# Kernel optimization log

Measured on AMD Instinct MI355X. Metric: run time of the kernel, lower is better.

The kernel has to match this reference:

```python
import jax, jax.numpy as jnp
from jax import lax
import numpy as np

B, EMB, HEADS, LAYERS = 32, 512, 8, 4
SEQ_JD, TOK = 200, 50

def _mask_lg(S):
    # Faithful vectorization of CoKEModel.mask_lg (True = masked)
    m = np.ones((B, HEADS, S, S), dtype=bool)
    rows = np.arange(S)[:, None]
    cols = np.clip(rows - 5 + np.arange(10)[None, :], 0, S - 1)  # window=10, offset -5..4
    for h in range(6):  # local_len = 6 local-window heads
        m[:, h, rows, cols] = False
    m[0, 6:] = False          # global heads unmasked only for batch 0 (faithful to source)
    m[:, :, 0, :] = False     # CLS row attends everywhere
    return m

def _ln_free(x):
    # CoKEModel.layer_norm: no affine, eps=1e-12, rsqrt form
    mu = jnp.mean(x, axis=-1, keepdims=True)
    sx = x - mu
    v = jnp.mean(sx * sx, axis=-1, keepdims=True)
    return sx * jnp.sqrt(1.0 / (v + 1e-12))

def _ln(x, g, b):
    mu = jnp.mean(x, axis=-1, keepdims=True)
    sx = x - mu
    v = jnp.mean(sx * sx, axis=-1, keepdims=True)
    return sx / jnp.sqrt(v + 1e-5) * g + b

def _textcnn(tokens, emb, cws, cbs, fw, fb):
    e = emb[tokens]                        # (N, 50, 1024)
    x = jnp.transpose(e, (0, 2, 1))        # (N, 1024, 50): embed dim as channels
    pooled = []
    for W, b in zip(cws, cbs):             # W: (100, k, 1024)
        rhs = jnp.transpose(W, (0, 2, 1))  # (100, 1024, k)
        y = lax.conv_general_dilated(x, rhs, (1,), 'VALID', dimension_numbers=('NCH', 'OIH', 'NCH'))
        y = jax.nn.relu(y + b[None, :, None])
        pooled.append(jnp.max(y, axis=2))  # global max-pool over time
    return jnp.concatenate(pooled, axis=1) @ fw.T + fb   # (N, 512)

def _encoder(x, mask, wq, bq, wk, bk, wv, bv, wo, bo, l1g, l1b, fw1, fb1, fw2, fb2, l2g, l2b):
    Bb, S, D = x.shape
    dh = D // HEADS
    scale = 1.0 / (dh ** 0.5)
    for l in range(LAYERS):
        q = (x @ wq[l].T + bq[l]).reshape(Bb, S, HEADS, dh)
        k = (x @ wk[l].T + bk[l]).reshape(Bb, S, HEADS, dh)
        v = (x @ wv[l].T + bv[l]).reshape(Bb, S, HEADS, dh)
        s = jnp.einsum('bshd,bthd->bhst', q, k) * scale
        s = jnp.where(mask, -1e9, s)
        a = jax.nn.softmax(s, axis=-1)
        c = jnp.einsum('bhst,bthd->bshd', a, v).reshape(Bb, S, D)
        x = _ln(x + c @ wo[l].T + bo[l], l1g[l], l1b[l])
        h = jax.nn.relu(x @ fw1[l].T + fb1[l])
        x = _ln(x + h @ fw2[l].T + fb2[l], l2g[l], l2b[l])
    return x

def _contrastive(im, s, margin=0.02):
    sc = im @ s.T
    d = jnp.diag(sc)
    cs = jnp.maximum(margin + sc - d[:, None], 0.0)
    ci = jnp.maximum(margin + sc - d[None, :], 0.0)
    eye = jnp.eye(sc.shape[0], dtype=bool)
    cs = jnp.where(eye, 0.0, cs)
    ci = jnp.where(eye, 0.0, ci)
    return jnp.sum(cs) + jnp.sum(ci)

def _forward(floats, src, mask101, mask200):
    (user_info, label_similarity, emb_tc, cw1, cb1, cw2, cb2, cw3, cb3, tfw, tfb,
     wq, bq, wk, bk, wv, bv, wo, bo, l1g, l1b, fw1, fb1, fw2, fb2, l2g, l2b,
     fc1w, fc1b, fc2w, fc2b, fc3w, fc3b, fc4w, fc4b, pscale, pbias) = floats
    cws, cbs = (cw1, cw2, cw3), (cb1, cb2, cb3)
    enc = (wq, bq, wk, bk, wv, bv, wo, bo, l1g, l1b, fw1, fb1, fw2, fb2, l2g, l2b)

    # ---- first pass: first 100 JDs + global CLS token ----
    s1 = _textcnn(src[:, :100].reshape(-1, TOK), emb_tc, cws, cbs, tfw, tfb).reshape(B, 100, EMB)
    s1 = _ln_free(s1)
    s1 = jnp.concatenate([jnp.zeros((B, 1, EMB), s1.dtype), s1], axis=1)  # (B, 101, EMB)
    p = _encoder(s1, mask101, *enc)
    p = jax.nn.gelu(p @ fc1w.T + fc1b, approximate=False)
    p = _ln_free(p)
    p = p * pscale[:, :p.shape[1]] + pbias[:, :p.shape[1]]
    p = p @ fc2w.T + fc2b                      # (B, 101, 204)
    cls_e, tok = p[:, :1], p[:, 1:]
    P = tok @ fc3w.T + fc3b                    # (B, 100, 204)
    clsIII = cls_e @ fc3w.T + fc3b             # (B, 1, 204)
    SLl = jnp.einsum('bsm,bsn->bmn', P, P)     # P^T @ P
    SL_hat = label_similarity[None] + 0.4 * SLl
    outIII = jnp.squeeze(clsIII @ SL_hat, axis=1)  # (B, 204)

    # ---- second pass: all 200 JDs ----
    s2 = _textcnn(src.reshape(-1, TOK), emb_tc, cws, cbs, tfw, tfb).reshape(B, SEQ_JD, EMB)
    s2 = _ln_free(s2)
    ap = _encoder(s2, mask200, *enc)
    ap = jax.nn.gelu(ap @ fc1w.T + fc1b, approximate=False)
    ap = _ln_free(ap)
    ap = ap * pscale[:, :SEQ_JD] + pbias[:, :SEQ_JD]
    p1 = ap @ fc2w.T + fc2b                    # (B, 200, 204)

    nn_ = SEQ_JD // 100  # = 2 neighbors
    eps = 1e-6
    skl_rows, seuc_rows = [], []
    for i in range(nn_):
        # NOTE: faithful to source slicing bug: [i : (i+1)*100]
        c1 = jax.nn.softmax(jnp.mean(p1[:, i:(i + 1) * 100], axis=1), axis=-1)
        a1 = jax.nn.softmax(jnp.mean(ap[:, i:(i + 1) * 100], axis=1), axis=-1)
        rk, re = [], []
        for j in range(nn_):
            c2 = jax.nn.softmax(jnp.mean(p1[:, j:(j + 1) * 100], axis=1), axis=-1)
            a2 = jax.nn.softmax(jnp.mean(ap[:, j:(j + 1) * 100], axis=1), axis=-1)
            rk.append(jnp.sum((c1 + eps) * jnp.log((c1 + eps) / (c2 + eps)), axis=-1))
            re.append(jnp.sqrt(jnp.sum((a1 - a2) ** 2, axis=-1) + 1e-12))
        skl_rows.append(jnp.stack(rk, axis=-1))
        seuc_rows.append(jnp.stack(re, axis=-1))
    skl = jnp.stack(skl_rows, axis=1).reshape(B, -1) * 10.0
    seuc = jnp.stack(seuc_rows, axis=1).reshape(B, -1)
    skl = jax.nn.softmax(skl, axis=-1)
    seuc = jax.nn.softmax(seuc, axis=-1)
    loss_sims = jnp.mean(jnp.sum((skl + eps) * jnp.log((skl + eps) / (seuc + eps)), axis=-1))

    cls4m = jnp.squeeze(cls_e, axis=1)
    user4m = user_info @ fc4w.T + fc4b
    nrm = lambda x: x / jnp.maximum(jnp.linalg.norm(x, axis=1, keepdims=True), 1e-12)
    match = _contrastive(nrm(cls4m), nrm(user4m))

    return (jax.nn.softmax(outIII, axis=-1),
            jax.nn.softmax(cls_e, axis=-1),
            loss_sims * 100000.0,
            match * 0.01)

def setup_inputs():
    key = jax.random.key(0)
    kit = iter(jax.random.split(key, 48))
    def nrm(shape, s=0.02):
        return jax.random.normal(next(kit), shape, jnp.float32) * s
    d = {}
    d['src'] = jax.random.randint(next(kit), (B, SEQ_JD, TOK), 0, 20000)
    d['user_info'] = nrm((B, 142), 1.0)
    d['label_similarity'] = nrm((204, 204))
    d['emb_tc'] = nrm((20000, 1024)).at[0].set(0.0)  # padding_idx=0 row zeroed
    d['cw1'], d['cb1'] = nrm((100, 1, 1024)), jnp.zeros((100,), jnp.float32)
    d['cw2'], d['cb2'] = nrm((100, 2, 1024)), jnp.zeros((100,), jnp.float32)
    d['cw3'], d['cb3'] = nrm((100, 3, 1024)), jnp.zeros((100,), jnp.float32)
    d['tfw'], d['tfb'] = nrm((512, 300)), jnp.zeros((512,), jnp.float32)
    d['wq'], d['bq'] = nrm((LAYERS, EMB, EMB)), jnp.zeros((LAYERS, EMB), jnp.float32)
    d['wk'], d['bk'] = nrm((LAYERS, EMB, EMB)), jnp.zeros((LAYERS, EMB), jnp.float32)
    d['wv'], d['bv'] = nrm((LAYERS, EMB, EMB)), jnp.zeros((LAYERS, EMB), jnp.float32)
    d['wo'], d['bo'] = nrm((LAYERS, EMB, EMB)), jnp.zeros((LAYERS, EMB), jnp.float32)
    d['l1g'], d['l1b'] = jnp.ones((LAYERS, EMB), jnp.float32), jnp.zeros((LAYERS, EMB), jnp.float32)
    d['fw1'], d['fb1'] = nrm((LAYERS, 2048, EMB)), jnp.zeros((LAYERS, 2048), jnp.float32)
    d['fw2'], d['fb2'] = nrm((LAYERS, EMB, 2048)), jnp.zeros((LAYERS, EMB), jnp.float32)
    d['l2g'], d['l2b'] = jnp.ones((LAYERS, EMB), jnp.float32), jnp.zeros((LAYERS, EMB), jnp.float32)
    d['fc1w'], d['fc1b'] = nrm((EMB, EMB)), jnp.zeros((EMB,), jnp.float32)
    d['fc2w'], d['fc2b'] = nrm((204, EMB)), jnp.zeros((204,), jnp.float32)
    d['fc3w'], d['fc3b'] = nrm((204, 204)), jnp.zeros((204,), jnp.float32)
    d['fc4w'], d['fc4b'] = nrm((204, 142)), jnp.zeros((204,), jnp.float32)
    d['pscale'] = jnp.ones((B, 300, EMB), jnp.float32)
    d['pbias'] = jnp.zeros((B, 300, EMB), jnp.float32)
    d['mask101'] = jnp.asarray(_mask_lg(101))
    d['mask200'] = jnp.asarray(_mask_lg(SEQ_JD))
    return d

def reference(src, user_info, label_similarity, emb_tc, cw1, cb1, cw2, cb2, cw3, cb3, tfw, tfb, wq, bq, wk, bk, wv, bv, wo, bo, l1g, l1b, fw1, fb1, fw2, fb2, l2g, l2b, fc1w, fc1b, fc2w, fc2b, fc3w, fc3b, fc4w, fc4b, pscale, pbias, mask101, mask200):
    floats = (user_info, label_similarity, emb_tc, cw1, cb1, cw2, cb2, cw3, cb3, tfw, tfb,
              wq, bq, wk, bk, wv, bv, wo, bo, l1g, l1b, fw1, fb1, fw2, fb2, l2g, l2b,
              fc1w, fc1b, fc2w, fc2b, fc3w, fc3b, fc4w, fc4b, pscale, pbias)
    return _forward(floats, src, mask101, mask200)
```

## Files before the change

kernel.cpp:

```cpp
#include <hip/hip_runtime.h>
#include <math.h>

#define EMB 512
#define HEADS 8
#define NLAYERS 4
#define NB 32
#define SEQ 200
#define TOKN 50
#define DH 64
#define FFND 2048
#define NCLS 204
#define VC 640
#define KD 1024
#define CCH 8
#define CROWS (6400/CCH)
#define CM (CROWS*TOKN)
#define MSEG 16
#define CMT ((CM + 127) / 128)
#define CNT (VC / 128)
#define CT  (CMT * CNT)

typedef __attribute__((ext_vector_type(8))) short v8s;
typedef __attribute__((ext_vector_type(4))) float v4f;
typedef unsigned short ushort_t;
// ... 449 lines not shown
        #pragma unroll
        for (int e = 0; e < 8; e++){
          int k = k0 + bkq + e;
          he[e] = (k < K) ? bph[k0 + e] : (ushort_t)0;
          le[e] = (k < K) ? bpl[k0 + e] : (ushort_t)0;
        }
        h0 = *(uint4*)&he[0];
        l0 = *(uint4*)&le[0];
      }
      *(uint4*)&Bhi[brow][bkq] = h0;
      *(uint4*)&Blo[brow][bkq] = l0;
    }
    __syncthreads();

    v8s ah[4], al[4];
    #pragma unroll
    for (int mi = 0; mi < 4; mi++){
      ah[mi] = *(const v8s*)&Ahi[wm + mi*16 + lcol][lq*8];
      al[mi] = *(const v8s*)&Alo[wm + mi*16 + lcol][lq*8];
    }
    #pragma unroll
    for (int ni = 0; ni < 2; ni++){
      v8s bh = *(const v8s*)&Bhi[wn + ni*16 + lcol][lq*8];
      v8s bl = *(const v8s*)&Blo[wn + ni*16 + lcol][lq*8];
      #pragma unroll
      for (int mi = 0; mi < 4; mi++){
        acc[mi][ni] = __builtin_amdgcn_mfma_f32_16x16x32_bf16(ah[mi], bh, acc[mi][ni], 0, 0, 0);
        acc[mi][ni] = __builtin_amdgcn_mfma_f32_16x16x32_bf16(al[mi], bh, acc[mi][ni], 0, 0, 0);
        acc[mi][ni] = __builtin_amdgcn_mfma_f32_16x16x32_bf16(ah[mi], bl, acc[mi][ni], 0, 0, 0);
      }
    }
    __syncthreads();
  }

  #pragma unroll
  for (int ni = 0; ni < 2; ni++){
    int n = n0 + wn + ni*16 + lcol;
    if (n >= N) continue;
    float bv = (ks == 1 || slice == 0) ? bias[n] : 0.f;
    #pragma unroll
    for (int mi = 0; mi < 4; mi++){
      int mbase = m0 + wm + mi*16 + lq*4;
      #pragma unroll
      for (int rg = 0; rg < 4; rg++){
        int m = mbase + rg;
        if (m >= M) continue;
        float v = acc[mi][ni][rg] + bv;
        if (ks == 1){
          if (act == 1) v = fmaxf(v, 0.f);
          else if (act == 2) v = 0.5f * v * (1.f + erff(v * 0.70710678118654752f));
          C[(size_t)m * ldc + n] = v;
        } else {
          atomicAdd(&C[(size_t)m * ldc + n], v);
        }
      }
    }
  }
}

__global__ __launch_bounds__(256, 2) void gemm_mfma_kernel(
    const float* __restrict__ A, const float* __restrict__ W,
    const float* __restrict__ bias, float* __restrict__ C,
    int M, int N, int K, int ldc, int act)
{
  __shared__ ushort_t Ahi[128][40];
  __shared__ ushort_t Alo[128][40];
  __shared__ ushort_t Bhi[128][40];
  __shared__ ushort_t Blo[128][40];

  const int tid = threadIdx.x;
  const int m0 = blockIdx.y * 128, n0 = blockIdx.x * 128;
  const int wave = tid >> 6, lane = tid & 63;
  const int wm = (wave >> 1) * 64, wn = (wave & 1) * 64;
  const int lcol = lane & 15, lq = lane >> 4;

  v4f acc[4][4];
  #pragma unroll
  for (int i = 0; i < 4; i++)
    #pragma unroll
    for (int j = 0; j < 4; j++) acc[i][j] = (v4f){0.f, 0.f, 0.f, 0.f};

  const int srow = tid >> 1;
  const int skh  = (tid & 1) * 16;

  for (int k0 = 0; k0 < K; k0 += 32){
    {
      float av[16];
      int m = m0 + srow;
      const float* ap = A + (size_t)m * K + k0 + skh;
      bool mok = (m < M);
      if (mok && (k0 + 32 <= K)){
        #pragma unroll
        for (int q = 0; q < 4; q++){
          float4 f = ((const float4*)ap)[q];
          av[q*4+0]=f.x; av[q*4+1]=f.y; av[q*4+2]=f.z; av[q*4+3]=f.w;
        }
      } else {
        #pragma unroll
        for (int e = 0; e < 16; e++){
          int k = k0 + skh + e;
          av[e] = (mok && k < K) ? ap[e] : 0.f;
        }
      }
      uint4 uh[2], ul[2];
      #pragma unroll
      for (int h = 0; h < 2; h++){
        unsigned hw[8], lw[8];
        #pragma unroll
        for (int e = 0; e < 8; e++){
          float x = av[h*8+e];
          unsigned u = __float_as_uint(x);
          float hf = __uint_as_float(u & 0xFFFF0000u);
          hw[e] = u >> 16;
          lw[e] = f2bu(x - hf);
        }
        uh[h] = make_uint4(hw[0]|(hw[1]<<16), hw[2]|(hw[3]<<16), hw[4]|(hw[5]<<16), hw[6]|(hw[7]<<16));
        ul[h] = make_uint4(lw[0]|(lw[1]<<16), lw[2]|(lw[3]<<16), lw[4]|(lw[5]<<16), lw[6]|(lw[7]<<16));
      }
      *(uint4*)&Ahi[srow][skh]     = uh[0];
      *(uint4*)&Ahi[srow][skh + 8] = uh[1];
      *(uint4*)&Alo[srow][skh]     = ul[0];
      *(uint4*)&Alo[srow][skh + 8] = ul[1];
    }
    {
      float bv[16];
      int n = n0 + srow;
      const float* bp = W + (size_t)n * K + k0 + skh;
      bool nok = (n < N);
      if (nok && (k0 + 32 <= K)){
        #pragma unroll
        for (int q = 0; q < 4; q++){
          float4 f = ((const float4*)bp)[q];
          bv[q*4+0]=f.x; bv[q*4+1]=f.y; bv[q*4+2]=f.z; bv[q*4+3]=f.w;
        }
      } else {
        #pragma unroll
        for (int e = 0; e < 16; e++){
          int k = k0 + skh + e;
          bv[e] = (nok && k < K) ? bp[e] : 0.f;
        }
      }
      uint4 uh[2], ul[2];
      #pragma unroll
      for (int h = 0; h < 2; h++){
        unsigned hw[8], lw[8];
        #pragma unroll
        for (int e = 0; e < 8; e++){
          float x = bv[h*8+e];
          unsigned u = __float_as_uint(x);
          float hf = __uint_as_float(u & 0xFFFF0000u);
          hw[e] = u >> 16;
          lw[e] = f2bu(x - hf);
        }
        uh[h] = make_uint4(hw[0]|(hw[1]<<16), hw[2]|(hw[3]<<16), hw[4]|(hw[5]<<16), hw[6]|(hw[7]<<16));
        ul[h] = make_uint4(lw[0]|(lw[1]<<16), lw[2]|(lw[3]<<16), lw[4]|(lw[5]<<16), lw[6]|(lw[7]<<16));
      }
      *(uint4*)&Bhi[srow][skh]     = uh[0];
      *(uint4*)&Bhi[srow][skh + 8] = uh[1];
      *(uint4*)&Blo[srow][skh]     = ul[0];
      *(uint4*)&Blo[srow][skh + 8] = ul[1];
    }
    __syncthreads();

    v8s ah[4], al[4];
    #pragma unroll
    for (int mi = 0; mi < 4; mi++){
      ah[mi] = *(const v8s*)&Ahi[wm + mi*16 + lcol][lq*8];
      al[mi] = *(const v8s*)&Alo[wm + mi*16 + lcol][lq*8];
    }
    #pragma unroll
    for (int ni = 0; ni < 4; ni++){
      v8s bh = *(const v8s*)&Bhi[wn + ni*16 + lcol][lq*8];
      v8s bl = *(const v8s*)&Blo[wn + ni*16 + lcol][lq*8];
      #pragma unroll
      for (int mi = 0; mi < 4; mi++){
        acc[mi][ni] = __builtin_amdgcn_mfma_f32_16x16x32_bf16(ah[mi], bh, acc[mi][ni], 0, 0, 0);
        acc[mi][ni] = __builtin_amdgcn_mfma_f32_16x16x32_bf16(al[mi], bh, acc[mi][ni], 0, 0, 0);
        acc[mi][ni] = __builtin_amdgcn_mfma_f32_16x16x32_bf16(ah[mi], bl, acc[mi][ni], 0, 0, 0);
      }
    }
    __syncthreads();
  }

  #pragma unroll
  for (int ni = 0; ni < 4; ni++){
    int n = n0 + wn + ni*16 + lcol;
    if (n >= N) continue;
    float bv = bias[n];
    #pragma unroll
    for (int mi = 0; mi < 4; mi++){
      int mbase = m0 + wm + mi*16 + lq*4;
      #pragma unroll
      for (int rg = 0; rg < 4; rg++){
        int m = mbase + rg;
        if (m >= M) continue;
        float v = acc[mi][ni][rg] + bv;
        if (act == 1) v = fmaxf(v, 0.f);
        else if (act == 2) v = 0.5f * v * (1.f + erff(v * 0.70710678118654752f));
        C[(size_t)m * ldc + n] = v;
      }
    }
  }
}

__global__ __launch_bounds__(256) void gemm_kernel(
    const float* __restrict__ A, const float* __restrict__ W,
    const float* __restrict__ bias, float* __restrict__ C,
    int M, int N, int K, int act)
{
  __shared__ float As[16][64];
  __shared__ float Ws[16][64];
  const int tid = threadIdx.x;
  const int m0 = blockIdx.y * 64, n0 = blockIdx.x * 64;
  const int lr = tid >> 2;
  const int lk = (tid & 3) * 4;
  const int tx = tid & 15, ty = tid >> 4;
  float cc[4][4];
  #pragma unroll
  for (int i = 0; i < 4; i++)
    #pragma unroll
    for (int j = 0; j < 4; j++) cc[i][j] = 0.f;

  for (int k0 = 0; k0 < K; k0 += 16){
    #pragma unroll
    for (int i = 0; i < 4; i++){
      int k = k0 + lk + i;
      int m = m0 + lr;
      As[lk + i][lr] = (m < M && k < K) ? A[(size_t)m * K + k] : 0.f;
      int n = n0 + lr;
      Ws[lk + i][lr] = (n < N && k < K) ? W[(size_t)n * K + k] : 0.f;
    }
    __syncthreads();
    #pragma unroll
    for (int kk = 0; kk < 16; kk++){
      float4 a = *(const float4*)&As[kk][ty * 4];
      float4 b = *(const float4*)&Ws[kk][tx * 4];
      float av[4] = {a.x, a.y, a.z, a.w};
      float bv[4] = {b.x, b.y, b.z, b.w};
      #pragma unroll
      for (int i = 0; i < 4; i++)
        #pragma unroll
        for (int j = 0; j < 4; j++) cc[i][j] = fmaf(av[i], bv[j], cc[i][j]);
    }
    __syncthreads();
  }

  #pragma unroll
  for (int i = 0; i < 4; i++){
    int m = m0 + ty * 4 + i;
    if (m >= M) continue;
    #pragma unroll
    for (int j = 0; j < 4; j++){
      int n = n0 + tx * 4 + j;
      if (n >= N) continue;
      float v = cc[i][j] + bias[n];
      if (act == 1) v = fmaxf(v, 0.f);
      else if (act == 2) v = 0.5f * v * (1.f + erff(v * 0.70710678118654752f));
      C[(size_t)m * N + n] = v;
    }
  }
}

__global__ __launch_bounds__(256) void ln_kernel(
    const float* __restrict__ X, const float* __restrict__ Res,
    const float* __restrict__ g, const float* __restrict__ bta,
    const float* __restrict__ pscale, const float* __restrict__ pbias,
    float* __restrict__ Y, int S, float eps)
{
  __shared__ float red[8];
  const int r = blockIdx.x, tid = threadIdx.x;
  size_t o0 = (size_t)r * EMB + tid;
  size_t o1 = o0 + 256;
  float v0 = X[o0] + (Res ? Res[o0] : 0.f);
  float v1 = X[o1] + (Res ? Res[o1] : 0.f);
  float tot = block_reduce(v0 + v1, red, 4, false);
  float mu = tot * (1.f / 512.f);
  float s0 = v0 - mu, s1 = v1 - mu;
  float var = block_reduce(s0 * s0 + s1 * s1, red, 4, false) * (1.f / 512.f);
  float rs = 1.f / sqrtf(var + eps);
  float y0 = s0 * rs, y1 = s1 * rs;
  if (g){
    y0 = y0 * g[tid] + bta[tid];
    y1 = y1 * g[tid + 256] + bta[tid + 256];
  }
  if (pscale){
    int b = r / S, t = r % S;
    size_t po = ((size_t)(b * 300 + t)) * EMB;
    y0 = y0 * pscale[po + tid] + pbias[po + tid];
    y1 = y1 * pscale[po + tid + 256] + pbias[po + tid + 256];
  }
  Y[o0] = y0;
  Y[o1] = y1;
}

__global__ __launch_bounds__(64) void vmean_kernel(const float* __restrict__ qkv,
                                                   float* __restrict__ vm, int S){
  int bh = blockIdx.x; int b = bh >> 3, h = bh & 7; int d = threadIdx.x;
  const float* vr = qkv + (size_t)(b * S) * 1536 + 1024 + h * DH + d;
  float s = 0.f;
  for (int j = 0; j < S; j++) s += vr[(size_t)j * 1536];
  vm[bh * DH + d] = s / (float)S;
}

__global__ __launch_bounds__(64) void attn_kernel(
    const float* __restrict__ qkv, const float* __restrict__ vm,
    float* __restrict__ Ctx, int S)
{
  __shared__ float qv[DH];
  __shared__ float sc[SEQ];
  __shared__ float wts[16];
  const int tid = threadIdx.x;
  const int blk = blockIdx.x;
  const int i = blk % S;
  const int bh = blk / S;
  const int h = bh % HEADS;
  const int b = bh / HEADS;
  const size_t rowoff = ((size_t)(b * S + i)) * 1536 + h * DH;
  const size_t coff = ((size_t)(b * S + i)) * EMB + h * DH;
  const bool rowall = (i == 0) || (b == 0 && h >= 6);

  if (rowall){
    qv[tid] = qkv[rowoff + tid];
    __syncthreads();
    for (int j = tid; j < S; j += 64){
      const float* kr = qkv + ((size_t)(b * S + j)) * 1536 + 512 + h * DH;
      float d = 0.f;
      #pragma unroll
      for (int d4 = 0; d4 < 16; d4++){
        float4 kk = *(const float4*)(kr + d4 * 4);
        d = fmaf(qv[d4*4+0], kk.x, d);
        d = fmaf(qv[d4*4+1], kk.y, d);
        d = fmaf(qv[d4*4+2], kk.z, d);
        d = fmaf(qv[d4*4+3], kk.w, d);
      }
      sc[j] = d * 0.125f;
    }
    __syncthreads();
    float mx = -INFINITY;
    for (int j = tid; j < S; j += 64) mx = fmaxf(mx, sc[j]);
    #pragma unroll
    for (int o = 32; o > 0; o >>= 1) mx = fmaxf(mx, __shfl_down(mx, o, 64));
    mx = __shfl(mx, 0, 64);
    float sm = 0.f;
    for (int j = tid; j < S; j += 64){ float e = expf(sc[j] - mx); sc[j] = e; sm += e; }
    #pragma unroll
    for (int o = 32; o > 0; o >>= 1) sm += __shfl_down(sm, o, 64);
    sm = __shfl(sm, 0, 64);
    float inv = 1.f / sm;
    __syncthreads();
    float a_ = 0.f;
    const float* vr = qkv + ((size_t)(b * S)) * 1536 + 1024 + h * DH + tid;
    for (int j = 0; j < S; j++) a_ = fmaf(sc[j], vr[(size_t)j * 1536], a_);
    Ctx[coff + tid] = a_ * inv;
  } else if (h < 6){
    qv[tid] = qkv[rowoff + tid];
    __syncthreads();
    const int lo = max(0, i - 5), hi = min(S - 1, i + 4);
    const int cnt = hi - lo + 1;
    float s = -INFINITY;
    if (tid < cnt){
      const float* kr = qkv + ((size_t)(b * S + lo + tid)) * 1536 + 512 + h * DH;
      float d = 0.f;
      #pragma unroll
      for (int d4 = 0; d4 < 16; d4++){
        float4 kk = *(const float4*)(kr + d4 * 4);
        d = fmaf(qv[d4*4+0], kk.x, d);
        d = fmaf(qv[d4*4+1], kk.y, d);
        d = fmaf(qv[d4*4+2], kk.z, d);
        d = fmaf(qv[d4*4+3], kk.w, d);
      }
      s = d * 0.125f;
    }
    float mx = s;
    #pragma unroll
    for (int o = 8; o > 0; o >>= 1) mx = fmaxf(mx, __shfl_xor(mx, o, 16));
    float e = (tid < cnt) ? expf(s - mx) : 0.f;
    float sm = e;
    #pragma unroll
    for (int o = 8; o > 0; o >>= 1) sm += __shfl_xor(sm, o, 16);
    if (tid < 16) wts[tid] = e / sm;
    __syncthreads();
    float a_ = 0.f;
    const float* vr = qkv + ((size_t)(b * S + lo)) * 1536 + 1024 + h * DH + tid;
    for (int j = 0; j < cnt; j++) a_ = fmaf(wts[j], vr[(size_t)j * 1536], a_);
    Ctx[coff + tid] = a_;
  } else {
    Ctx[coff + tid] = vm[(b * HEADS + h) * DH + tid];
  }
}

__global__ void buildx1_kernel(const float* __restrict__ base, float* __restrict__ x1){
  int idx = blockIdx.x * 256 + threadIdx.x;
  if (idx >= NB * 101 * EMB) return;
  int e = idx & 511;
  int bt = idx >> 9;
  int t = bt % 101, b = bt / 101;
  x1[idx] = (t == 0) ? 0.f : base[((size_t)(b * SEQ + t - 1)) * EMB + e];
}

__global__ void extract_kernel(const float* __restrict__ p2, float* __restrict__ clsE, float* __restrict__ tok){
  int idx = blockIdx.x * 256 + threadIdx.x;
  if (idx >= NB * 101 * NCLS) return;
  int n = idx % NCLS;
  int bt = idx / NCLS;
  int t = bt % 101, b = bt / 101;
  float v = p2[idx];
  if (t == 0) clsE[b * NCLS + n] = v;
  else tok[((size_t)(b * 100 + t - 1)) * NCLS + n] = v;
}

__global__ void zero_kernel(float* p){ if (threadIdx.x == 0) p[0] = 0.f; }

__global__ __launch_bounds__(256) void slhat_kernel(
    const float* __restrict__ P, const float* __restrict__ ls, float* __restrict__ SLh)
{
  int bm = blockIdx.x;
  int b = bm / NCLS, m = bm % NCLS;
  int n = threadIdx.x;
  if (n >= NCLS) return;
  const float* Pb = P + (size_t)b * 100 * NCLS;
  float s = 0.f;
  for (int t = 0; t < 100; t++) s = fmaf(Pb[t * NCLS + m], Pb[t * NCLS + n], s);
  SLh[((size_t)bm) * NCLS + n] = ls[m * NCLS + n] + 0.4f * s;
}

__global__ __launch_bounds__(256) void outIII_kernel(
    const float* __restrict__ cls3, const float* __restrict__ SLh, float* __restrict__ o3)
{
  int b = blockIdx.x, n = threadIdx.x;
  if (n >= NCLS) return;
  float s = 0.f;
  for (int m = 0; m < NCLS; m++)
    s = fmaf(cls3[b * NCLS + m], SLh[((size_t)(b * NCLS + m)) * NCLS + n], s);
  o3[b * NCLS + n] = s;
}

__global__ __launch_bounds__(256) void softmax_out_kernel(const float* __restrict__ X, float* __restrict__ O, int n){
  __shared__ float red[8];
  int r = blockIdx.x, tid = threadIdx.x;
  float mx = -INFINITY;
  for (int j = tid; j < n; j += 256) mx = fmaxf(mx, X[(size_t)r * n + j]);
  mx = block_reduce(mx, red, 4, true);
  float sm = 0.f;
  for (int j = tid; j < n; j += 256) sm += expf(X[(size_t)r * n + j] - mx);
  sm = block_reduce(sm, red, 4, false);
  for (int j = tid; j < n; j += 256) O[(size_t)r * n + j] = expf(X[(size_t)r * n + j] - mx) / sm;
}

__global__ __launch_bounds__(256) void normalize_kernel(
    const float* __restrict__ clsE, const float* __restrict__ u4,
    float* __restrict__ imn, float* __restrict__ sn)
{
  __shared__ float red[8];
  int r = blockIdx.x, tid = threadIdx.x;
  const float* s = (r < NB) ? (clsE + (size_t)r * NCLS) : (u4 + (size_t)(r - NB) * NCLS);
  float* d = (r < NB) ? (imn + (size_t)r * NCLS) : (sn + (size_t)(r - NB) * NCLS);
  float v = (tid < NCLS) ? s[tid] : 0.f;
  float ss = block_reduce(v * v, red, 4, false);
  float nrm = fmaxf(sqrtf(ss), 1e-12f);
  if (tid < NCLS) d[tid] = v / nrm;
}

__global__ __launch_bounds__(1024) void contrastive_kernel(
    const float* __restrict__ imn, const float* __restrict__ sn, float* __restrict__ out)
{
  __shared__ float sc[NB][NB];
  __shared__ float red[16];
  int tid = threadIdx.x;
  int i = tid >> 5, j = tid & 31;
  float d = 0.f;
  for (int c = 0; c < NCLS; c++) d = fmaf(imn[i * NCLS + c], sn[j * NCLS + c], d);
  sc[i][j] = d;
  __syncthreads();
  float di = sc[i][i], dj = sc[j][j];
  float v = 0.f;
  if (i != j)
    v = fmaxf(0.02f + sc[i][j] - di, 0.f) + fmaxf(0.02f + sc[i][j] - dj, 0.f);
  #pragma unroll
  for (int o = 32; o > 0; o >>= 1) v += __shfl_down(v, o, 64);
  if ((tid & 63) == 0) red[tid >> 6] = v;
  __syncthreads();
  if (tid == 0){
    float s = 0.f;
    for (int w = 0; w < 16; w++) s += red[w];
    out[13057] = s * 0.01f;
  }
}

__global__ __launch_bounds__(256) void means_part_kernel(
    const float* __restrict__ p1, const float* __restrict__ ap,
    float* __restrict__ part)
{
  const int blk = blockIdx.x;
  const int bi = blk / MSEG, seg = blk % MSEG;
  const int b = bi >> 1, i = bi & 1;
  const int start = i;
  const int cnt = (i == 0) ? 100 : 199;
  const int per = (cnt + MSEG - 1) / MSEG;
  const int r0 = seg * per;
  const int r1 = min(r0 + per, cnt);
  float* dst = part + (size_t)blk * 720;
  for (int c = threadIdx.x; c < NCLS + EMB; c += 256){
    float s = 0.f;
    if (c < NCLS){
      for (int rr = r0; rr < r1; rr++)
        s += p1[((size_t)(b * SEQ + start + rr)) * NCLS + c];
    } else {
      int cc = c - NCLS;
      for (int rr = r0; rr < r1; rr++)
        s += ap[((size_t)(b * SEQ + start + rr)) * EMB + cc];
    }
    dst[c] = s;
  }
}

__global__ __launch_bounds__(256) void means_final_kernel(
    const float* __restrict__ part, float* __restrict__ mp, float* __restrict__ ma)
{
  const int bi = blockIdx.x;
  const int i = bi & 1;
  const float icnt = (i == 0) ? (1.f / 100.f) : (1.f / 199.f);
  for (int c = threadIdx.x; c < NCLS + EMB; c += 256){
    float s = 0.f;
    #pragma unroll
    for (int g = 0; g < MSEG; g++)
      s += part[((size_t)(bi * MSEG + g)) * 720 + c];
    if (c < NCLS) mp[(size_t)bi * NCLS + c] = s * icnt;
    else          ma[(size_t)bi * EMB + (c - NCLS)] = s * icnt;
  }
}

__global__ __launch_bounds__(64) void klfinal_kernel(
    const float* __restrict__ cbuf, const float* __restrict__ abuf, float* __restrict__ acc)
{
  const int b = blockIdx.x, lane = threadIdx.x;
  float rk[4], re[4];
  #pragma unroll
  for (int pr = 0; pr < 4; pr++){
    int i = pr >> 1, j = pr & 1;
    const float* c1 = cbuf + ((size_t)(b * 2 + i)) * NCLS;
    const float* c2 = cbuf + ((size_t)(b * 2 + j)) * NCLS;
    float s = 0.f;
    for (int n = lane; n < NCLS; n += 64){
      float x = c1[n] + 1e-6f, y = c2[n] + 1e-6f;
      s += x * logf(x / y);
    }
    #pragma unroll
    for (int o = 32; o > 0; o >>= 1) s += __shfl_down(s, o, 64);
    rk[pr] = __shfl(s, 0, 64);
    const float* a1 = abuf + ((size_t)(b * 2 + i)) * EMB;
    const float* a2 = abuf + ((size_t)(b * 2 + j)) * EMB;
    float s2 = 0.f;
    for (int n = lane; n < EMB; n += 64){
      float dd = a1[n] - a2[n];
      s2 += dd * dd;
    }
    #pragma unroll
    for (int o = 32; o > 0; o >>= 1) s2 += __shfl_down(s2, o, 64);
    re[pr] = sqrtf(__shfl(s2, 0, 64) + 1e-12f);
  }
  if (lane == 0){
    float sk[4], se[4];
    float mk = -INFINITY, me = -INFINITY;
    for (int p = 0; p < 4; p++){
      sk[p] = rk[p] * 10.f;
      mk = fmaxf(mk, sk[p]);
      se[p] = re[p];
      me = fmaxf(me, se[p]);
    }
    float ssk = 0.f, sse = 0.f;
    for (int p = 0; p < 4; p++){ sk[p] = expf(sk[p] - mk); ssk += sk[p]; se[p] = expf(se[p] - me); sse += se[p]; }
    float loss = 0.f;
    for (int p = 0; p < 4; p++){
      float x = sk[p] / ssk + 1e-6f, y = se[p] / sse + 1e-6f;
      loss += x * logf(x / y);
    }
    atomicAdd(acc, loss);
  }
}

__global__ void finalize_kernel(const float* __restrict__ acc, float* __restrict__ out){
  if (threadIdx.x == 0) out[13056] = acc[0] * (100000.f / 32.f);
}

extern "C" void kernel_launch(void* const* d_in, const int* in_sizes, int n_in,
                              void* d_out, int out_size, void* d_ws, size_t ws_size,
                              hipStream_t stream)
{
  (void)in_sizes; (void)n_in; (void)out_size;
  const int*   src  = (const int*)  d_in[0];
  const float* user_info = (const float*)d_in[1];
  const float* ls   = (const float*)d_in[2];
  const float* emb  = (const float*)d_in[3];
  const float* cw1  = (const float*)d_in[4];  const float* cb1 = (const float*)d_in[5];
  const float* cw2  = (const float*)d_in[6];  const float* cb2 = (const float*)d_in[7];
  const float* cw3  = (const float*)d_in[8];  const float* cb3 = (const float*)d_in[9];
  const float* tfw  = (const float*)d_in[10]; const float* tfb = (const float*)d_in[11];
  const float* wq   = (const float*)d_in[12]; const float* bq  = (const float*)d_in[13];
  const float* wk   = (const float*)d_in[14]; const float* bk  = (const float*)d_in[15];
  const float* wv   = (const float*)d_in[16]; const float* bv  = (const float*)d_in[17];
  const float* wo   = (const float*)d_in[18]; const float* bo  = (const float*)d_in[19];
  const float* l1g  = (const float*)d_in[20]; const float* l1b = (const float*)d_in[21];
  const float* fw1  = (const float*)d_in[22]; const float* fb1 = (const float*)d_in[23];
  const float* fw2  = (const float*)d_in[24]; const float* fb2 = (const float*)d_in[25];
  const float* l2g  = (const float*)d_in[26]; const float* l2b = (const float*)d_in[27];
  const float* fc1w = (const float*)d_in[28]; const float* fc1b= (const float*)d_in[29];
  const float* fc2w = (const float*)d_in[30]; const float* fc2b= (const float*)d_in[31];
  const float* fc3w = (const float*)d_in[32]; const float* fc3b= (const float*)d_in[33];
  const float* fc4w = (const float*)d_in[34]; const float* fc4b= (const float*)d_in[35];
  const float* pscale = (const float*)d_in[36];
  const float* pbias  = (const float*)d_in[37];
  float* out = (float*)d_out;
  float* ws = (float*)d_ws;

  size_t off = 0;
  auto alloc = [&](size_t n){ float* p = ws + off; off += ((n + 3) & ~(size_t)3); return p; };
  float* base = alloc(6400ULL * EMB);
  float* x1   = alloc((size_t)NB * 101 * EMB);
  float* qkv  = alloc(6400ULL * 1536);
  float* ctx  = alloc(6400ULL * EMB);
  float* proj = alloc(6400ULL * EMB);
  float* hb   = alloc(6400ULL * FFND);
  float* p2   = alloc(6400ULL * NCLS);
  float* clsE = alloc((size_t)NB * NCLS);
  float* tok  = alloc(3200ULL * NCLS);
  float* Pb   = alloc(3200ULL * NCLS);
  float* cls3 = alloc((size_t)NB * NCLS);
  float* SLh  = alloc((size_t)NB * NCLS * NCLS);
  float* o3   = alloc((size_t)NB * NCLS);
  float* u4   = alloc((size_t)NB * NCLS);
  float* imn  = alloc((size_t)NB * NCLS);
  float* sn   = alloc((size_t)NB * NCLS);
  float* mp   = alloc(64ULL * NCLS);
  float* ma   = alloc(64ULL * EMB);
  float* cbf  = alloc(64ULL * NCLS);
  float* abf  = alloc(64ULL * EMB);
  float* lacc = alloc(4);
  float* vmb  = alloc((size_t)NB * HEADS * DH);
  ushort_t* Wb = (ushort_t*)alloc((size_t)VC * KD / 2);
  float* tfwT = alloc(300ULL * EMB);
  float* bqkv = alloc(4ULL * 1536);
  ushort_t* embb = (ushort_t*)qkv;
  const size_t OQKV = 0, OWO = 3145728, OF1 = 4194304, OF2 = 8388608;
  const size_t OC1 = 12582912, OC2 = 12845056, OC3 = 12949504, WTOT = 12991120;
  ushort_t* WhiA = (ushort_t*)alloc((WTOT + 1) / 2);
  ushort_t* WloA = (ushort_t*)alloc((WTOT + 1) / 2);
  const bool presplit = (off * sizeof(float) <= ws_size);

  auto gemm_f32 = [&](const float* A, const float* W, const float* bi, float* C,
                      int M, int N, int K, int act){
    dim3 g((N + 63) / 64, (M + 63) / 64);
    gemm_kernel<<<g, 256, 0, stream>>>(A, W, bi, C, M, N, K, act);
  };
  auto gemm_fly = [&](const float* A, const float* W, const float* bi, float* C,
                      int M, int N, int K, int ldc, int act){
    dim3 g((N + 127) / 128, (M + 127) / 128);
    gemm_mfma_kernel<<<g, 256, 0, stream>>>(A, W, bi, C, M, N, K, ldc, act);
  };
  auto gemm_pre = [&](const float* A, size_t woff, const float* bi, float* C,
                      int M, int N, int K, int ldc, int act){
    int mt = (M + 127) / 128;
    if (N <= 512){
      int nt = (N + 63) / 64;
      int tiles = mt * nt;
      int ks = 1;
      if (act == 0){
        while (ks < 8 && tiles * ks * 2 <= 2048 && K / (ks * 2) >= 128) ks *= 2;
      }
      if (ks > 1){
        size_t n4 = ((size_t)M * N) / 4;
        int zg = (int)min((n4 + 255) / 256, (size_t)2048);
        zerobuf_kernel<<<zg, 256, 0, stream>>>(C, n4);
      }
      gemm_mfma_pre64_kernel<<<tiles * ks, 256, 0, stream>>>(
          A, WhiA + woff, WloA + woff, bi, C, M, N, K, ldc, act, mt, nt, ks);
    } else {
      int nt = (N + 127) / 128;
      gemm_mfma_pre_kernel<<<mt * nt, 256, 0, stream>>>(
          A, WhiA + woff, WloA + woff, bi, C, M, N, K, ldc, act, mt, nt);
    }
  };
  auto split = [&](const float* srcw, size_t woff, int n){
    split_kernel<<<(n / 4 + 255) / 256, 256, 0, stream>>>(srcw, WhiA + woff, WloA + woff, n);
  };

  prep_w_kernel<<<(VC * KD / 4 + 255) / 256, 256, 0, stream>>>(cw1, cw2, cw3, Wb);
  prep_embbf_kernel<<<(int)((20000ULL * KD / 4 + 255) / 256), 256, 0, stream>>>(emb, embb);
  prep_tfwT_kernel<<<(300 * EMB + 255) / 256, 256, 0, stream>>>(tfw, tfwT);
  if (presplit){
    for (int l = 0; l < NLAYERS; l++){
      split(wq + (size_t)l * 262144, OQKV + (size_t)l * 786432,          262144);
      split(wk + (size_t)l * 262144, OQKV + (size_t)l * 786432 + 262144, 262144);
      split(wv + (size_t)l * 262144, OQKV + (size_t)l * 786432 + 524288, 262144);
      split(wo + (size_t)l * 262144, OWO + (size_t)l * 262144, 262144);
      split(fw1 + (size_t)l * 1048576, OF1 + (size_t)l * 1048576, 1048576);
      split(fw2 + (size_t)l * 1048576, OF2 + (size_t)l * 1048576, 1048576);
    }
    split(fc1w, OC1, 262144);
    split(fc2w, OC2, NCLS * EMB);
    split(fc3w, OC3, NCLS * NCLS);
    qkvbias_kernel<<<4, 256, 0, stream>>>(bq, bk, bv, bqkv);
  }

  for (int c = 0; c < CCH; c++){
    conv_gemm_kernel<<<CT, 256, 0, stream>>>(
        src + (size_t)c * CM, embb, Wb, (ushort_t*)hb, CM);
    pool_fc_kernel<<<CROWS, 256, 0, stream>>>(
        (ushort_t*)hb, tfwT, cb1, cb2, cb3, tfb, base + (size_t)c * CROWS * EMB);
  }
  buildx1_kernel<<<(NB * 101 * EMB + 255) / 256, 256, 0, stream>>>(base, x1);

  auto encoder = [&](float* x, int S){
    int M = NB * S;
    for (int l = 0; l < NLAYERS; l++){
      if (presplit){
        gemm_pre(x, OQKV + (size_t)l * 786432, bqkv + l * 1536, qkv, M, 1536, EMB, 1536, 0);
      } else {
        gemm_fly(x, wq + (size_t)l * EMB * EMB, bq + l * EMB, qkv,        M, EMB, EMB, 1536, 0);
        gemm_fly(x, wk + (size_t)l * EMB * EMB, bk + l * EMB, qkv + 512,  M, EMB, EMB, 1536, 0);
        gemm_fly(x, wv + (size_t)l * EMB * EMB, bv + l * EMB, qkv + 1024, M, EMB, EMB, 1536, 0);
      }
      vmean_kernel<<<NB * HEADS, 64, 0, stream>>>(qkv, vmb, S);
      attn_kernel<<<NB * HEADS * S, 64, 0, stream>>>(qkv, vmb, ctx, S);
      if (presplit) gemm_pre(ctx, OWO + (size_t)l * 262144, bo + l * EMB, proj, M, EMB, EMB, EMB, 0);
      else gemm_fly(ctx, wo + (size_t)l * EMB * EMB, bo + l * EMB, proj, M, EMB, EMB, EMB, 0);
      ln_kernel<<<M, 256, 0, stream>>>(proj, x, l1g + l * EMB, l1b + l * EMB, nullptr, nullptr, x, S, 1e-5f);
      if (presplit) gemm_pre(x, OF1 + (size_t)l * 1048576, fb1 + l * FFND, hb, M, FFND, EMB, FFND, 1);
      else gemm_fly(x, fw1 + (size_t)l * FFND * EMB, fb1 + l * FFND, hb, M, FFND, EMB, FFND, 1);
      if (presplit) gemm_pre(hb, OF2 + (size_t)l * 1048576, fb2 + l * EMB, proj, M, EMB, FFND, EMB, 0);
      else gemm_fly(hb, fw2 + (size_t)l * EMB * FFND, fb2 + l * EMB, proj, M, EMB, FFND, EMB, 0);
      ln_kernel<<<M, 256, 0, stream>>>(proj, x, l2g + l * EMB, l2b + l * EMB, nullptr, nullptr, x, S, 1e-5f);
    }
    if (presplit) gemm_pre(x, OC1, fc1b, ctx, M, EMB, EMB, EMB, 2);
    else gemm_fly(x, fc1w, fc1b, ctx, M, EMB, EMB, EMB, 2);
    ln_kernel<<<M, 256, 0, stream>>>(ctx, nullptr, nullptr, nullptr, pscale, pbias, ctx, S, 1e-12f);
    if (presplit) gemm_pre(ctx, OC2, fc2b, p2, M, NCLS, EMB, NCLS, 0);
    else gemm_fly(ctx, fc2w, fc2b, p2, M, NCLS, EMB, NCLS, 0);
  };

  encoder(x1, 101);
  extract_kernel<<<(NB * 101 * NCLS + 255) / 256, 256, 0, stream>>>(p2, clsE, tok);
  if (presplit) gemm_pre(tok, OC3, fc3b, Pb, 3200, NCLS, NCLS, NCLS, 0);
  else gemm_fly(tok, fc3w, fc3b, Pb, 3200, NCLS, NCLS, NCLS, 0);
  gemm_f32(clsE, fc3w, fc3b, cls3, NB, NCLS, NCLS, 0);
  slhat_kernel<<<NB * NCLS, 256, 0, stream>>>(Pb, ls, SLh);
  outIII_kernel<<<NB, 256, 0, stream>>>(cls3, SLh, o3);
  softmax_out_kernel<<<NB, 256, 0, stream>>>(o3, out, NCLS);
  softmax_out_kernel<<<NB, 256, 0, stream>>>(clsE, out + NB * NCLS, NCLS);
  gemm_f32(user_info, fc4w, fc4b, u4, NB, NCLS, 142, 0);
  normalize_kernel<<<64, 256, 0, stream>>>(clsE, u4, imn, sn);
  contrastive_kernel<<<1, 1024, 0, stream>>>(imn, sn, out);

  encoder(base, SEQ);
  zero_kernel<<<1, 64, 0, stream>>>(lacc);
  means_part_kernel<<<64 * MSEG, 256, 0, stream>>>(p2, ctx, hb);
  means_final_kernel<<<64, 256, 0, stream>>>(hb, mp, ma);
  softmax_out_kernel<<<64, 256, 0, stream>>>(mp, cbf, NCLS);
  softmax_out_kernel<<<64, 256, 0, stream>>>(ma, abf, EMB);
  klfinal_kernel<<<NB, 64, 0, stream>>>(cbf, abf, lacc);
  finalize_kernel<<<1, 64, 0, stream>>>(lacc, out);
}
```

Before: 5.308 ms.

## Split attention into full-row, banded, and mean-fill kernels; limit split-K to large K

The single divergent attention kernel is split into three specialised kernels. One handles the rows that attend to every position (CLS rows, plus the global heads of batch 0). One handles the local 10-wide window with one wavefront per row, four rows per block, keeping scores in registers and reducing dot products with cross-lane shuffles. The third copies the precomputed V-mean for masked global-head rows. This removes block-level branch divergence and the many tiny 64-thread blocks, at the cost of two extra launches per layer. Split-K in the small-N GEMM path is now restricted to K>=1024, which avoids the zero-fill kernel and atomic accumulation for the K=512 GEMMs.

```diff
diff --git a/kernel.cpp b/kernel.cpp
--- a/kernel.cpp
+++ b/kernel.cpp
@@ -775,91 +775,108 @@
   vm[bh * DH + d] = s / (float)S;
 }
 
-__global__ __launch_bounds__(64) void attn_kernel(
-    const float* __restrict__ qkv, const float* __restrict__ vm,
-    float* __restrict__ Ctx, int S)
+__global__ __launch_bounds__(64) void attn_full_kernel(
+    const float* __restrict__ qkv, float* __restrict__ Ctx, int S)
 {
   __shared__ float qv[DH];
   __shared__ float sc[SEQ];
-  __shared__ float wts[16];
   const int tid = threadIdx.x;
   const int blk = blockIdx.x;
-  const int i = blk % S;
-  const int bh = blk / S;
-  const int h = bh % HEADS;
-  const int b = bh / HEADS;
+  int b, h, i;
+  if (blk < NB * HEADS){ b = blk >> 3; h = blk & 7; i = 0; }
+  else {
+    int idx = blk - NB * HEADS;
+    b = 0; h = 6 + idx / (S - 1); i = 1 + idx % (S - 1);
+  }
   const size_t rowoff = ((size_t)(b * S + i)) * 1536 + h * DH;
   const size_t coff = ((size_t)(b * S + i)) * EMB + h * DH;
-  const bool rowall = (i == 0) || (b == 0 && h >= 6);
-
-  if (rowall){
-    qv[tid] = qkv[rowoff + tid];
-    __syncthreads();
-    for (int j = tid; j < S; j += 64){
-      const float* kr = qkv + ((size_t)(b * S + j)) * 1536 + 512 + h * DH;
-      float d = 0.f;
-      #pragma unroll
-      for (int d4 = 0; d4 < 16; d4++){
-        float4 kk = *(const float4*)(kr + d4 * 4);
-        d = fmaf(qv[d4*4+0], kk.x, d);
-        d = fmaf(qv[d4*4+1], kk.y, d);
-        d = fmaf(qv[d4*4+2], kk.z, d);
-        d = fmaf(qv[d4*4+3], kk.w, d);
-      }
-      sc[j] = d * 0.125f;
-    }
-    __syncthreads();
-    float mx = -INFINITY;
-    for (int j = tid; j < S; j += 64) mx = fmaxf(mx, sc[j]);
-    #pragma unroll
-    for (int o = 32; o > 0; o >>= 1) mx = fmaxf(mx, __shfl_down(mx, o, 64));
-    mx = __shfl(mx, 0, 64);
-    float sm = 0.f;
-    for (int j = tid; j < S; j += 64){ float e = expf(sc[j] - mx); sc[j] = e; sm += e; }
-    #pragma unroll
-    for (int o = 32; o > 0; o >>= 1) sm += __shfl_down(sm, o, 64);
-    sm = __shfl(sm, 0, 64);
-    float inv = 1.f / sm;
-    __syncthreads();
-    float a_ = 0.f;
-    const float* vr = qkv + ((size_t)(b * S)) * 1536 + 1024 + h * DH + tid;
-    for (int j = 0; j < S; j++) a_ = fmaf(sc[j], vr[(size_t)j * 1536], a_);
-    Ctx[coff + tid] = a_ * inv;
-  } else if (h < 6){
-    qv[tid] = qkv[rowoff + tid];
-    __syncthreads();
-    const int lo = max(0, i - 5), hi = min(S - 1, i + 4);
-    const int cnt = hi - lo + 1;
-    float s = -INFINITY;
-    if (tid < cnt){
-      const float* kr = qkv + ((size_t)(b * S + lo + tid)) * 1536 + 512 + h * DH;
-      float d = 0.f;
-      #pragma unroll
-      for (int d4 = 0; d4 < 16; d4++){
-        float4 kk = *(const float4*)(kr + d4 * 4);
-        d = fmaf(qv[d4*4+0], kk.x, d);
-        d = fmaf(qv[d4*4+1], kk.y, d);
-        d = fmaf(qv[d4*4+2], kk.z, d);
-        d = fmaf(qv[d4*4+3], kk.w, d);
-      }
-      s = d * 0.125f;
-    }
-    float mx = s;
-    #pragma unroll
-    for (int o = 8; o > 0; o >>= 1) mx = fmaxf(mx, __shfl_xor(mx, o, 16));
-    float e = (tid < cnt) ? expf(s - mx) : 0.f;
-    float sm = e;
-    #pragma unroll
-    for (int o = 8; o > 0; o >>= 1) sm += __shfl_xor(sm, o, 16);
-    if (tid < 16) wts[tid] = e / sm;
-    __syncthreads();
-    float a_ = 0.f;
-    const float* vr = qkv + ((size_t)(b * S + lo)) * 1536 + 1024 + h * DH + tid;
-    for (int j = 0; j < cnt; j++) a_ = fmaf(wts[j], vr[(size_t)j * 1536], a_);
-    Ctx[coff + tid] = a_;
-  } else {
-    Ctx[coff + tid] = vm[(b * HEADS + h) * DH + tid];
-  }
+
+  qv[tid] = qkv[rowoff + tid];
+  __syncthreads();
+  for (int j = tid; j < S; j += 64){
+    const float* kr = qkv + ((size_t)(b * S + j)) * 1536 + 512 + h * DH;
+    float d = 0.f;
+    #pragma unroll
+    for (int d4 = 0; d4 < 16; d4++){
+      float4 kk = *(const float4*)(kr + d4 * 4);
+      d = fmaf(qv[d4*4+0], kk.x, d);
+      d = fmaf(qv[d4*4+1], kk.y, d);
+      d = fmaf(qv[d4*4+2], kk.z, d);
+      d = fmaf(qv[d4*4+3], kk.w, d);
+    }
+    sc[j] = d * 0.125f;
+  }
+  __syncthreads();
+  float mx = -INFINITY;
+  for (int j = tid; j < S; j += 64) mx = fmaxf(mx, sc[j]);
+  #pragma unroll
+  for (int o = 32; o > 0; o >>= 1) mx = fmaxf(mx, __shfl_down(mx, o, 64));
+  mx = __shfl(mx, 0, 64);
+  float sm = 0.f;
+  for (int j = tid; j < S; j += 64){ float e = expf(sc[j] - mx); sc[j] = e; sm += e; }
+  #pragma unroll
+  for (int o = 32; o > 0; o >>= 1) sm += __shfl_down(sm, o, 64);
+  sm = __shfl(sm, 0, 64);
+  float inv = 1.f / sm;
+  __syncthreads();
+  float a_ = 0.f;
+  const float* vr = qkv + ((size_t)(b * S)) * 1536 + 1024 + h * DH + tid;
+  for (int j = 0; j < S; j++) a_ = fmaf(sc[j], vr[(size_t)j * 1536], a_);
+  Ctx[coff + tid] = a_ * inv;
+}
+
+__global__ __launch_bounds__(256) void attn_band_kernel(
+    const float* __restrict__ qkv, float* __restrict__ Ctx, int S)
+{
+  const int rows = NB * 6 * (S - 1);
+  const int r = blockIdx.x * 4 + (threadIdx.x >> 6);
+  const int lane = threadIdx.x & 63;
+  if (r >= rows) return;
+  const int i = 1 + r % (S - 1);
+  const int q_ = r / (S - 1);
+  const int h = q_ % 6, b = q_ / 6;
+  const float* base = qkv + (size_t)(b * S) * 1536;
+  const float qd = base[(size_t)i * 1536 + h * DH + lane];
+  const int lo = max(0, i - 5), hi = min(S - 1, i + 4);
+  const int cnt = hi - lo + 1;
+
+  float sc_r[10];
+  #pragma unroll
+  for (int jj = 0; jj < 10; jj++){
+    float p = 0.f;
+    if (jj < cnt) p = qd * base[(size_t)(lo + jj) * 1536 + 512 + h * DH + lane];
+    #pragma unroll
+    for (int o = 32; o > 0; o >>= 1) p += __shfl_xor(p, o, 64);
+    sc_r[jj] = (jj < cnt) ? p * 0.125f : -INFINITY;
+  }
+  float mx = sc_r[0];
+  #pragma unroll
+  for (int jj = 1; jj < 10; jj++) mx = fmaxf(mx, sc_r[jj]);
+  float sm = 0.f;
+  #pragma unroll
+  for (int jj = 0; jj < 10; jj++){ sc_r[jj] = expf(sc_r[jj] - mx); sm += sc_r[jj]; }
+  const float inv = 1.f / sm;
+  float a_ = 0.f;
+  #pragma unroll
+  for (int jj = 0; jj < 10; jj++){
+    if (jj < cnt) a_ = fmaf(sc_r[jj], base[(size_t)(lo + jj) * 1536 + 1024 + h * DH + lane], a_);
+  }
+  Ctx[((size_t)(b * S + i)) * EMB + h * DH + lane] = a_ * inv;
+}
+
+__global__ __launch_bounds__(256) void vmfill_kernel(
+    const float* __restrict__ vm, float* __restrict__ Ctx, int S)
+{
+  const int total = (NB - 1) * 2 * (S - 1) * 64;
+  int idx = blockIdx.x * 256 + threadIdx.x;
+  if (idx >= total) return;
+  const int d = idx & 63;
+  int rest = idx >> 6;
+  const int i = 1 + rest % (S - 1);
+  rest /= (S - 1);
+  const int h = 6 + (rest & 1);
+  const int b = 1 + (rest >> 1);
+  Ctx[((size_t)(b * S + i)) * EMB + h * DH + d] = vm[(b * HEADS + h) * DH + d];
 }
 
 __global__ void buildx1_kernel(const float* __restrict__ base, float* __restrict__ x1){
@@ -1137,7 +1154,7 @@
       int nt = (N + 63) / 64;
       int tiles = mt * nt;
       int ks = 1;
-      if (act == 0){
+      if (act == 0 && K >= 1024){
         while (ks < 8 && tiles * ks * 2 <= 2048 && K / (ks * 2) >= 128) ks *= 2;
       }
       if (ks > 1){
@@ -1194,7 +1211,9 @@
         gemm_fly(x, wv + (size_t)l * EMB * EMB, bv + l * EMB, qkv + 1024, M, EMB, EMB, 1536, 0);
       }
       vmean_kernel<<<NB * HEADS, 64, 0, stream>>>(qkv, vmb, S);
-      attn_kernel<<<NB * HEADS * S, 64, 0, stream>>>(qkv, vmb, ctx, S);
+      attn_full_kernel<<<NB * HEADS + 2 * (S - 1), 64, 0, stream>>>(qkv, ctx, S);
+      attn_band_kernel<<<(NB * 6 * (S - 1) + 3) / 4, 256, 0, stream>>>(qkv, ctx, S);
+      vmfill_kernel<<<((NB - 1) * 2 * (S - 1) * 64 + 255) / 256, 256, 0, stream>>>(vmb, ctx, S);
       if (presplit) gemm_pre(ctx, OWO + (size_t)l * 262144, bo + l * EMB, proj, M, EMB, EMB, EMB, 0);
       else gemm_fly(ctx, wo + (size_t)l * EMB * EMB, bo + l * EMB, proj, M, EMB, EMB, EMB, 0);
       ln_kernel<<<M, 256, 0, stream>>>(proj, x, l1g + l * EMB, l1b + l * EMB, nullptr, nullptr, x, S, 1e-5f);
```

After: 4.968 ms. 6.4% less time.
